# Kernel tuning notes

Measured on AMD Instinct MI355X. Metric: run time of the kernel, lower is better.

Reference implementation:

```python
import jax, jax.numpy as jnp
import numpy as np

CUTOFF = 5.0
NIPSIN = 3
NELE = 4        # natomtype
NWAVE = 10      # ntype: radial params per element
NB, NA, NEIGH = 1, 12000, 64
NPAIR = NA * NEIGH
# index_para: maps 12 angular components (3 p + 9 d) to order index 0/1
INDEX_PARA = np.concatenate([np.full(3 ** i, i - 1, dtype=np.int32) for i in range(1, NIPSIN)])
NANG = INDEX_PARA.shape[0]  # 12


def setup_inputs() -> dict:
    key = jax.random.key(0)
    ks = jax.random.split(key, 8)
    coordinates = jax.random.normal(ks[0], (NB, NA, 3), dtype=jnp.float32)
    numatoms = NA
    atom_index = jax.random.randint(ks[1], (2, NB, NPAIR), 0, NA)
    shifts = jax.random.normal(ks[2], (NB, NPAIR, 3), dtype=jnp.float32) * 0.1
    species = jax.random.randint(ks[3], (NB * NA,), 0, NELE)
    rs = jax.random.uniform(ks[4], (NELE, NWAVE), dtype=jnp.float32) * 4.0
    inta = jax.random.uniform(ks[5], (NELE, NWAVE), dtype=jnp.float32) + 0.2
    params = jax.random.uniform(ks[6], (NELE,), dtype=jnp.float32) * 0.5 + 0.5
    return {"coordinates": coordinates, "numatoms": numatoms, "atom_index": atom_index,
            "shifts": shifts, "species": species, "rs": rs, "inta": inta, "params": params}


def _density(coordinates, atom_index, shifts, species, rs, inta):
    nb, na, _ = coordinates.shape
    coords = coordinates.reshape(-1, 3)
    totnatom = coords.shape[0]
    npair = atom_index.shape[2]
    # flatten pair index lists with per-molecule atom offset (faithful for nb=1)
    ai = jnp.transpose(atom_index, (1, 0, 2)).reshape(2, -1)                 # (2, nb*npair)
    off = jnp.broadcast_to((jnp.arange(nb) * na)[:, None], (nb, npair)).reshape(-1)
    idx12 = ai + off[None, :]
    shift_v = shifts.reshape(-1, 3)
    valid = jnp.all(shift_v > -1e9, axis=-1)                                 # padding mask (all True here)
    dist_vec = coords[idx12[0]] - coords[idx12[1]] + shift_v                 # (P,3)
    d = jnp.linalg.norm(dist_vec, axis=-1)                                   # (P,)
    sp = species[idx12[0]]                                                   # (P,)
    # radial Gaussian * cosine cutoff, params gathered per center-atom type
    fcut = 0.5 * (jnp.cos(jnp.pi * jnp.minimum(d / CUTOFF, 1.0)) + 1.0)
    radial = jnp.exp(-10.0 * inta[sp] * jnp.square(d[:, None] - rs[sp])) * fcut[:, None]
    radial = jnp.where(valid[:, None], radial, 0.0)                          # (P, NWAVE)
    # angular outer products of unit vectors: p (3) then d (9)
    u = dist_vec / d[:, None]
    orbs = []
    orb = jnp.ones((u.shape[0], 1), dtype=u.dtype)
    for _ in range(1, NIPSIN):
        orb = (orb[:, :, None] * u[:, None, :]).reshape(u.shape[0], -1)
        orbs.append(orb)
    angular = jnp.concatenate(orbs, axis=1)                                  # (P, NANG)
    # scatter-reduce into per-(atom, neighbor-type) accumulators, then square
    seg = idx12[0] * NELE + sp
    rd = jax.ops.segment_sum(radial, seg, num_segments=totnatom * NELE)
    rd = jnp.square(rd).reshape(totnatom, NELE, NWAVE)
    oa = (angular[:, :, None] * radial[:, None, :]).reshape(u.shape[0], -1)  # (P, NANG*NWAVE)
    ad = jax.ops.segment_sum(oa, seg, num_segments=totnatom * NELE)
    ad = jnp.square(ad).reshape(totnatom, NELE, NANG, NWAVE)
    # contract angular components of the same order (index_para)
    acc = jnp.zeros((totnatom, NELE, NIPSIN - 1, NWAVE), dtype=ad.dtype)
    acc = acc.at[:, :, jnp.asarray(INDEX_PARA), :].add(ad)
    return jnp.concatenate([rd, acc.reshape(totnatom, NELE, -1)], axis=2)    # (T, NELE, 30)


def reference(coordinates, numatoms, atom_index, shifts, species, rs, inta, params):
    density = _density(coordinates, atom_index, shifts, species, rs, inta)
    density_w = density * params[None, :, None]                 # einsum('ijk,j->ijk')
    g = jnp.einsum('ilj,imj->ijlm', density_w, density_w)       # (T, nfeat, NELE, NELE)
    return jnp.sqrt(g).reshape(g.shape[0], g.shape[1], -1).sum(-1)  # (T, nfeat)
```

## Files before the change

### kernel.cpp

```cpp
#include <hip/hip_runtime.h>
#include <math.h>

#define NA 12000
#define NPAIR 768000
#define NWAVE 10
#define BINS 256
#define APB 47
#define BCAP 4096
#define RCAP 3584
#define PPB 3072

__global__ __launch_bounds__(512) void bin_kernel(
        const float* __restrict__ coords,
        const int* __restrict__ ai0,
        const int* __restrict__ ai1,
        const float* __restrict__ shifts,
        unsigned int* __restrict__ cursor,
        float4* __restrict__ records,
        unsigned char* __restrict__ aloc8) {
    __shared__ unsigned int hist[BINS];
    __shared__ unsigned int gbase[BINS];

    int tid = threadIdx.x;
    if (tid < BINS) hist[tid] = 0u;
    __syncthreads();

    float4 recr[6];
    unsigned int meta[6];
    int pbase = blockIdx.x * PPB;
    #pragma unroll
    for (int r = 0; r < 6; r++) {
        int p  = pbase + r * 512 + tid;
        int a  = ai0[p];
        int j  = ai1[p];
        float sx = shifts[3 * p + 0];
        float sy = shifts[3 * p + 1];
        float sz = shifts[3 * p + 2];
        float dx = coords[3 * a + 0] - coords[3 * j + 0] + sx;
        float dy = coords[3 * a + 1] - coords[3 * j + 1] + sy;
        float dz = coords[3 * a + 2] - coords[3 * j + 2] + sz;
        float d  = sqrtf(dx * dx + dy * dy + dz * dz);
        float tt = fminf(d * 0.2f, 1.0f);
        float fcut = 0.5f * __cosf(3.14159265358979f * tt) + 0.5f;
        if (!((sx > -1e9f) && (sy > -1e9f) && (sz > -1e9f))) fcut = 0.0f;
        unsigned int bin  = (unsigned int)a / 47u;
        unsigned int aloc = (unsigned int)a - bin * 47u;
        recr[r] = make_float4(dx, dy, dz, fcut);
        unsigned int rk = atomicAdd(&hist[bin], 1u);
        meta[r] = (bin << 18) | (aloc << 12) | rk;
    }
    __syncthreads();

    if (tid < BINS) gbase[tid] = atomicAdd(&cursor[tid], hist[tid]);
    __syncthreads();

    #pragma unroll
    for (int r = 0; r < 6; r++) {
        unsigned int bin  = meta[r] >> 18;
        unsigned int aloc = (meta[r] >> 12) & 63u;
        unsigned int gr   = gbase[bin] + (meta[r] & 0xFFFu);
        if (gr < BCAP) {
            unsigned int dg = bin * BCAP + gr;
            records[dg] = recr[r];
            aloc8[dg] = (unsigned char)aloc;
        }
    }
}

__global__ __launch_bounds__(512) void accum_kernel(
        const float4* __restrict__ records,
        const unsigned char* __restrict__ aloc8,
        const int*    __restrict__ species,
        const float*  __restrict__ params,
        const float*  __restrict__ rs,
        const float*  __restrict__ inta,
        const unsigned int* __restrict__ cursor,
        float* __restrict__ out) {
    __shared__ unsigned short idx[RCAP];
    __shared__ float spart[8][APB * 101];
    __shared__ unsigned int hist[APB];
    __shared__ unsigned int offs[APB];
    __shared__ int spl[APB];

    int tid  = threadIdx.x;
    int wv   = tid >> 6;
    int lane = tid & 63;
    int bin  = blockIdx.x;

    if (tid < APB) {
        hist[tid] = 0u;
        int ag = bin * APB + tid;
        spl[tid] = (ag < NA) ? species[ag] : 0;
    }
    __syncthreads();

    unsigned int cnt = cursor[bin];
    if (cnt > RCAP) cnt = RCAP;
    unsigned int base = (unsigned int)bin * BCAP;

    unsigned int pend[7];
    #pragma unroll
    for (int r = 0; r < 7; r++) {
        unsigned int k = (unsigned int)(r * 512 + tid);
        pend[r] = 0xFFFFFFFFu;
        if (k < cnt) {
            unsigned int aloc = aloc8[base + k];
            unsigned int rk = atomicAdd(&hist[aloc], 1u);
            pend[r] = (aloc << 20) | (rk << 12) | k;
        }
    }
    __syncthreads();

    if (wv == 0) {
        unsigned int h0 = (lane < APB) ? hist[lane] : 0u;
        unsigned int h = h0;
        #pragma unroll
        for (int s = 1; s < 64; s <<= 1) {
            unsigned int v = __shfl_up(h, s, 64);
            if (lane >= s) h += v;
        }
        if (lane < APB) offs[lane] = h - h0;
    }
    __syncthreads();

    #pragma unroll
    for (int r = 0; r < 7; r++) {
        if (pend[r] != 0xFFFFFFFFu) {
            unsigned int aloc = pend[r] >> 20;
            unsigned int rk   = (pend[r] >> 12) & 0xFFu;
            unsigned int k    = pend[r] & 0xFFFu;
            idx[offs[aloc] + rk] = (unsigned short)k;
        }
    }
    __syncthreads();

    if (lane < APB) {
        int a = lane;
        unsigned int offa = offs[a];
        unsigned int cnta = hist[a];
        int sp = spl[a];
        float trs[10], tin[10];
        #pragma unroll
        for (int w = 0; w < 10; w++) {
            trs[w] = rs[sp * NWAVE + w];
            tin[w] = -10.0f * inta[sp * NWAVE + w];
        }

        float S[10], P[30], D[60];
        #pragma unroll
        for (int w = 0; w < 10; w++) S[w] = 0.0f;
        #pragma unroll
        for (int c = 0; c < 30; c++) P[c] = 0.0f;
        #pragma unroll
        for (int c = 0; c < 60; c++) D[c] = 0.0f;

        for (unsigned int j = (unsigned int)wv; j < cnta; j += 8) {
            unsigned int k = idx[offa + j];
            float4 rec = records[base + k];
            float fcut = rec.w;
            float d2 = rec.x * rec.x + rec.y * rec.y + rec.z * rec.z;
            float dinv = rsqrtf(fmaxf(d2, 1e-24f));
            float d  = d2 * dinv;
            float ux = rec.x * dinv, uy = rec.y * dinv, uz = rec.z * dinv;
            float uxx = ux * ux, uxy = ux * uy, uxz = ux * uz;
            float uyy = uy * uy, uyz = uy * uz, uzz = uz * uz;
            #pragma unroll
            for (int w = 0; w < 10; w++) {
                float dr = d - trs[w];
                float r  = __expf(tin[w] * dr * dr) * fcut;
                S[w]      += r;
                P[w]      += ux  * r;
                P[10 + w] += uy  * r;
                P[20 + w] += uz  * r;
                D[w]      += uxx * r;
                D[10 + w] += uxy * r;
                D[20 + w] += uxz * r;
                D[30 + w] += uyy * r;
                D[40 + w] += uyz * r;
                D[50 + w] += uzz * r;
            }
        }

        float* row = &spart[wv][a * 101];
        #pragma unroll
        for (int w = 0; w < 10; w++) row[w]      = S[w];
        #pragma unroll
        for (int c = 0; c < 30; c++) row[10 + c] = P[c];
        #pragma unroll
        for (int c = 0; c < 60; c++) row[40 + c] = D[c];
    }
    __syncthreads();

    for (int i = tid; i < APB * 101; i += 512) {
        float s = spart[0][i] + spart[1][i] + spart[2][i] + spart[3][i]
                + spart[4][i] + spart[5][i] + spart[6][i] + spart[7][i];
        spart[0][i] = s;
    }
    __syncthreads();

    for (int v = tid; v < APB * 30; v += 512) {
        int atom = v / 30;
        int c = v - atom * 30;
        int ag = bin * APB + atom;
        if (ag < NA) {
            float pr = params[spl[atom]];
            const float* ap = &spart[0][atom * 101];
            float o;
            if (c < 10) {
                float s = ap[c];
                o = pr * s * s;
            } else if (c < 20) {
                int w = c - 10;
                float a1 = ap[10 + w], b1 = ap[20 + w], c1 = ap[30 + w];
                o = pr * (a1 * a1 + b1 * b1 + c1 * c1);
            } else {
                int w = c - 20;
                float xx = ap[40 + w], xy = ap[50 + w], xz = ap[60 + w];
                float yy = ap[70 + w], yz = ap[80 + w], zz = ap[90 + w];
                o = pr * (xx * xx + yy * yy + zz * zz
                          + 2.0f * (xy * xy + xz * xz + yz * yz));
            }
            out[ag * 30 + c] = o;
        }
    }
}


extern "C" void kernel_launch(void* const* d_in, const int* in_sizes, int n_in,
                              void* d_out, int out_size, void* d_ws, size_t ws_size,
                              hipStream_t stream) {
    const float* coords  = (const float*)d_in[0];
    const int*   aidx    = (const int*)d_in[2];
    const float* shifts  = (const float*)d_in[3];
    const int*   species = (const int*)d_in[4];
    const float* rs      = (const float*)d_in[5];
    const float* inta    = (const float*)d_in[6];
    const float* params  = (const float*)d_in[7];
    float* out = (float*)d_out;

    char* ws = (char*)d_ws;
    float4*        records = (float4*)(ws);
    unsigned int*  cursor  = (unsigned int*)(ws + 16777216);
    unsigned char* aloc8   = (unsigned char*)(ws + 16778240);

    const int* ai0 = aidx;
    const int* ai1 = aidx + NPAIR;

    hipMemsetAsync(cursor, 0, BINS * sizeof(unsigned int), stream);
    bin_kernel<<<NPAIR / PPB, 512, 0, stream>>>(coords, ai0, ai1, shifts,
                                                cursor, records, aloc8);
    accum_kernel<<<BINS, 512, 0, stream>>>(records, aloc8, species, params,
                                           rs, inta, cursor, out);
}
```

Baseline: 111.4 us.

## Sort records by bin in shared memory before global scatter for coalesced writes

The binning kernel now stages each block's computed pair records in LDS, computes an exclusive prefix over the per-bin histogram, and builds a permutation so records are written to global memory in bin-sorted order. Consecutive threads then write contiguous runs within each bin segment, replacing a random scatter of float4 and byte stores. The cost is about 73KB of extra shared memory per block, which lowers occupancy, plus extra barriers and a scan step.

Result: slower. 122.1 us (+9.6%).

```diff
diff --git a/kernel.cpp b/kernel.cpp
--- a/kernel.cpp
+++ b/kernel.cpp
@@ -19,18 +19,23 @@
         float4* __restrict__ records,
         unsigned char* __restrict__ aloc8) {
     __shared__ unsigned int hist[BINS];
+    __shared__ unsigned int excl[BINS];
     __shared__ unsigned int gbase[BINS];
+    __shared__ float4 stage[PPB];
+    __shared__ unsigned char salo[PPB];
+    __shared__ unsigned short inv[PPB];
+    __shared__ unsigned int dest[PPB];
 
     int tid = threadIdx.x;
     if (tid < BINS) hist[tid] = 0u;
     __syncthreads();
 
-    float4 recr[6];
-    unsigned int meta[6];
+    unsigned int binr[6], rankr[6];
     int pbase = blockIdx.x * PPB;
     #pragma unroll
     for (int r = 0; r < 6; r++) {
-        int p  = pbase + r * 512 + tid;
+        int li = r * 512 + tid;
+        int p  = pbase + li;
         int a  = ai0[p];
         int j  = ai1[p];
         float sx = shifts[3 * p + 0];
@@ -45,24 +50,59 @@
         if (!((sx > -1e9f) && (sy > -1e9f) && (sz > -1e9f))) fcut = 0.0f;
         unsigned int bin  = (unsigned int)a / 47u;
         unsigned int aloc = (unsigned int)a - bin * 47u;
-        recr[r] = make_float4(dx, dy, dz, fcut);
+        stage[li] = make_float4(dx, dy, dz, fcut);
+        salo[li]  = (unsigned char)aloc;
         unsigned int rk = atomicAdd(&hist[bin], 1u);
-        meta[r] = (bin << 18) | (aloc << 12) | rk;
-    }
-    __syncthreads();
-
-    if (tid < BINS) gbase[tid] = atomicAdd(&cursor[tid], hist[tid]);
+        binr[r] = bin;
+        rankr[r] = rk;
+    }
+    __syncthreads();
+
+    if (tid < 64) {
+        int l = tid;
+        unsigned int h0 = hist[4 * l + 0];
+        unsigned int h1 = hist[4 * l + 1];
+        unsigned int h2 = hist[4 * l + 2];
+        unsigned int h3 = hist[4 * l + 3];
+        unsigned int mysum = h0 + h1 + h2 + h3;
+        unsigned int incl = mysum;
+        #pragma unroll
+        for (int s = 1; s < 64; s <<= 1) {
+            unsigned int v = __shfl_up(incl, s, 64);
+            if (l >= s) incl += v;
+        }
+        unsigned int b = incl - mysum;
+        excl[4 * l + 0] = b;
+        excl[4 * l + 1] = b + h0;
+        excl[4 * l + 2] = b + h0 + h1;
+        excl[4 * l + 3] = b + h0 + h1 + h2;
+        gbase[4 * l + 0] = atomicAdd(&cursor[4 * l + 0], h0);
+        gbase[4 * l + 1] = atomicAdd(&cursor[4 * l + 1], h1);
+        gbase[4 * l + 2] = atomicAdd(&cursor[4 * l + 2], h2);
+        gbase[4 * l + 3] = atomicAdd(&cursor[4 * l + 3], h3);
+    }
     __syncthreads();
 
     #pragma unroll
     for (int r = 0; r < 6; r++) {
-        unsigned int bin  = meta[r] >> 18;
-        unsigned int aloc = (meta[r] >> 12) & 63u;
-        unsigned int gr   = gbase[bin] + (meta[r] & 0xFFFu);
-        if (gr < BCAP) {
-            unsigned int dg = bin * BCAP + gr;
-            records[dg] = recr[r];
-            aloc8[dg] = (unsigned char)aloc;
+        int li = r * 512 + tid;
+        unsigned int s  = excl[binr[r]] + rankr[r];
+        unsigned int gr = gbase[binr[r]] + rankr[r];
+        inv[s]  = (unsigned short)li;
+        dest[s] = (gr < BCAP) ? (binr[r] * BCAP + gr) : 0xFFFFFFFFu;
+    }
+    __syncthreads();
+
+    #pragma unroll
+    for (int r = 0; r < 6; r++) {
+        int s = r * 512 + tid;
+        int li = inv[s];
+        unsigned int dg = dest[s];
+        float4 rec = stage[li];
+        unsigned char al = salo[li];
+        if (dg != 0xFFFFFFFFu) {
+            records[dg] = rec;
+            aloc8[dg] = al;
         }
     }
 }
```

## Fuse binning and accumulation into one cooperative kernel with grid syncs

Applied to the files above, without the earlier changes.

Merges the memset, binning kernel and accumulation kernel into a single cooperative launch of 256 blocks. A grid-wide sync separates cursor zeroing, binning and accumulation, and the two phases share LDS through a union. Pairs per block change to 3000 so that 256 blocks cover all pairs. This removes two launch gaps and the memset, but adds grid-sync cost. Binning now runs on 256 blocks instead of 250, and occupancy is pinned to one block per CU.

Result: slower. 250.2 us (+124.5%).

```diff
diff --git a/kernel.cpp b/kernel.cpp
--- a/kernel.cpp
+++ b/kernel.cpp
@@ -1,5 +1,8 @@
 #include <hip/hip_runtime.h>
+#include <hip/hip_cooperative_groups.h>
 #include <math.h>
+
+namespace cg = cooperative_groups;
 
 #define NA 12000
 #define NPAIR 768000
@@ -8,89 +11,100 @@
 #define APB 47
 #define BCAP 4096
 #define RCAP 3584
-#define PPB 3072
-
-__global__ __launch_bounds__(512) void bin_kernel(
+#define PPB 3000
+
+struct S1 { unsigned int hist[BINS]; unsigned int gbase[BINS]; };
+struct S2 {
+    unsigned short idx[RCAP];
+    float spart[8][APB * 101];
+    unsigned int hist[APB];
+    unsigned int offs[APB];
+    int spl[APB];
+};
+union SMem { S1 s1; S2 s2; };
+
+__global__ __launch_bounds__(512, 1) void fused_kernel(
         const float* __restrict__ coords,
         const int* __restrict__ ai0,
         const int* __restrict__ ai1,
         const float* __restrict__ shifts,
+        const int* __restrict__ species,
+        const float* __restrict__ params,
+        const float* __restrict__ rs,
+        const float* __restrict__ inta,
         unsigned int* __restrict__ cursor,
         float4* __restrict__ records,
-        unsigned char* __restrict__ aloc8) {
-    __shared__ unsigned int hist[BINS];
-    __shared__ unsigned int gbase[BINS];
-
-    int tid = threadIdx.x;
-    if (tid < BINS) hist[tid] = 0u;
+        unsigned char* __restrict__ aloc8,
+        float* __restrict__ out) {
+    __shared__ SMem sm;
+    cg::grid_group grid = cg::this_grid();
+
+    int tid  = threadIdx.x;
+    int blk  = blockIdx.x;
+    int wv   = tid >> 6;
+    int lane = tid & 63;
+
+    if (tid == 0) cursor[blk] = 0u;
+    grid.sync();
+
+    if (tid < BINS) sm.s1.hist[tid] = 0u;
     __syncthreads();
 
     float4 recr[6];
     unsigned int meta[6];
-    int pbase = blockIdx.x * PPB;
+    int pbase = blk * PPB;
     #pragma unroll
     for (int r = 0; r < 6; r++) {
-        int p  = pbase + r * 512 + tid;
-        int a  = ai0[p];
-        int j  = ai1[p];
-        float sx = shifts[3 * p + 0];
-        float sy = shifts[3 * p + 1];
-        float sz = shifts[3 * p + 2];
-        float dx = coords[3 * a + 0] - coords[3 * j + 0] + sx;
-        float dy = coords[3 * a + 1] - coords[3 * j + 1] + sy;
-        float dz = coords[3 * a + 2] - coords[3 * j + 2] + sz;
-        float d  = sqrtf(dx * dx + dy * dy + dz * dz);
-        float tt = fminf(d * 0.2f, 1.0f);
-        float fcut = 0.5f * __cosf(3.14159265358979f * tt) + 0.5f;
-        if (!((sx > -1e9f) && (sy > -1e9f) && (sz > -1e9f))) fcut = 0.0f;
-        unsigned int bin  = (unsigned int)a / 47u;
-        unsigned int aloc = (unsigned int)a - bin * 47u;
-        recr[r] = make_float4(dx, dy, dz, fcut);
-        unsigned int rk = atomicAdd(&hist[bin], 1u);
-        meta[r] = (bin << 18) | (aloc << 12) | rk;
-    }
-    __syncthreads();
-
-    if (tid < BINS) gbase[tid] = atomicAdd(&cursor[tid], hist[tid]);
+        int li = r * 512 + tid;
+        meta[r] = 0xFFFFFFFFu;
+        if (li < PPB) {
+            int p  = pbase + li;
+            int a  = ai0[p];
+            int j  = ai1[p];
+            float sx = shifts[3 * p + 0];
+            float sy = shifts[3 * p + 1];
+            float sz = shifts[3 * p + 2];
+            float dx = coords[3 * a + 0] - coords[3 * j + 0] + sx;
+            float dy = coords[3 * a + 1] - coords[3 * j + 1] + sy;
+            float dz = coords[3 * a + 2] - coords[3 * j + 2] + sz;
+            float d  = sqrtf(dx * dx + dy * dy + dz * dz);
+            float tt = fminf(d * 0.2f, 1.0f);
+            float fcut = 0.5f * __cosf(3.14159265358979f * tt) + 0.5f;
+            if (!((sx > -1e9f) && (sy > -1e9f) && (sz > -1e9f))) fcut = 0.0f;
+            unsigned int bin  = (unsigned int)a / 47u;
+            unsigned int aloc = (unsigned int)a - bin * 47u;
+            recr[r] = make_float4(dx, dy, dz, fcut);
+            unsigned int rk = atomicAdd(&sm.s1.hist[bin], 1u);
+            meta[r] = (bin << 18) | (aloc << 12) | rk;
+        }
+    }
+    __syncthreads();
+
+    if (tid < BINS) sm.s1.gbase[tid] = atomicAdd(&cursor[tid], sm.s1.hist[tid]);
     __syncthreads();
 
     #pragma unroll
     for (int r = 0; r < 6; r++) {
-        unsigned int bin  = meta[r] >> 18;
-        unsigned int aloc = (meta[r] >> 12) & 63u;
-        unsigned int gr   = gbase[bin] + (meta[r] & 0xFFFu);
-        if (gr < BCAP) {
-            unsigned int dg = bin * BCAP + gr;
-            records[dg] = recr[r];
-            aloc8[dg] = (unsigned char)aloc;
-        }
-    }
-}
-
-__global__ __launch_bounds__(512) void accum_kernel(
-        const float4* __restrict__ records,
-        const unsigned char* __restrict__ aloc8,
-        const int*    __restrict__ species,
-        const float*  __restrict__ params,
-        const float*  __restrict__ rs,
-        const float*  __restrict__ inta,
-        const unsigned int* __restrict__ cursor,
-        float* __restrict__ out) {
-    __shared__ unsigned short idx[RCAP];
-    __shared__ float spart[8][APB * 101];
-    __shared__ unsigned int hist[APB];
-    __shared__ unsigned int offs[APB];
-    __shared__ int spl[APB];
-
-    int tid  = threadIdx.x;
-    int wv   = tid >> 6;
-    int lane = tid & 63;
-    int bin  = blockIdx.x;
-
+        if (meta[r] != 0xFFFFFFFFu) {
+            unsigned int bin  = meta[r] >> 18;
+            unsigned int aloc = (meta[r] >> 12) & 63u;
+            unsigned int gr   = sm.s1.gbase[bin] + (meta[r] & 0xFFFu);
+            if (gr < BCAP) {
+                unsigned int dg = bin * BCAP + gr;
+                records[dg] = recr[r];
+                aloc8[dg] = (unsigned char)aloc;
+            }
+        }
+    }
+
+    __threadfence();
+    grid.sync();
+
+    int bin = blk;
     if (tid < APB) {
-        hist[tid] = 0u;
+        sm.s2.hist[tid] = 0u;
         int ag = bin * APB + tid;
-        spl[tid] = (ag < NA) ? species[ag] : 0;
+        sm.s2.spl[tid] = (ag < NA) ? species[ag] : 0;
     }
     __syncthreads();
 
@@ -105,21 +119,21 @@
         pend[r] = 0xFFFFFFFFu;
         if (k < cnt) {
             unsigned int aloc = aloc8[base + k];
-            unsigned int rk = atomicAdd(&hist[aloc], 1u);
+            unsigned int rk = atomicAdd(&sm.s2.hist[aloc], 1u);
             pend[r] = (aloc << 20) | (rk << 12) | k;
         }
     }
     __syncthreads();
 
     if (wv == 0) {
-        unsigned int h0 = (lane < APB) ? hist[lane] : 0u;
+        unsigned int h0 = (lane < APB) ? sm.s2.hist[lane] : 0u;
         unsigned int h = h0;
         #pragma unroll
         for (int s = 1; s < 64; s <<= 1) {
             unsigned int v = __shfl_up(h, s, 64);
             if (lane >= s) h += v;
         }
-        if (lane < APB) offs[lane] = h - h0;
+        if (lane < APB) sm.s2.offs[lane] = h - h0;
     }
     __syncthreads();
 
@@ -129,16 +143,16 @@
             unsigned int aloc = pend[r] >> 20;
             unsigned int rk   = (pend[r] >> 12) & 0xFFu;
             unsigned int k    = pend[r] & 0xFFFu;
-            idx[offs[aloc] + rk] = (unsigned short)k;
+            sm.s2.idx[sm.s2.offs[aloc] + rk] = (unsigned short)k;
         }
     }
     __syncthreads();
 
     if (lane < APB) {
         int a = lane;
-        unsigned int offa = offs[a];
-        unsigned int cnta = hist[a];
-        int sp = spl[a];
+        unsigned int offa = sm.s2.offs[a];
+        unsigned int cnta = sm.s2.hist[a];
+        int sp = sm.s2.spl[a];
         float trs[10], tin[10];
         #pragma unroll
         for (int w = 0; w < 10; w++) {
@@ -155,7 +169,7 @@
         for (int c = 0; c < 60; c++) D[c] = 0.0f;
 
         for (unsigned int j = (unsigned int)wv; j < cnta; j += 8) {
-            unsigned int k = idx[offa + j];
+            unsigned int k = sm.s2.idx[offa + j];
             float4 rec = records[base + k];
             float fcut = rec.w;
             float d2 = rec.x * rec.x + rec.y * rec.y + rec.z * rec.z;
@@ -181,7 +195,7 @@
             }
         }
 
-        float* row = &spart[wv][a * 101];
+        float* row = &sm.s2.spart[wv][a * 101];
         #pragma unroll
         for (int w = 0; w < 10; w++) row[w]      = S[w];
         #pragma unroll
@@ -192,9 +206,9 @@
     __syncthreads();
 
     for (int i = tid; i < APB * 101; i += 512) {
-        float s = spart[0][i] + spart[1][i] + spart[2][i] + spart[3][i]
-                + spart[4][i] + spart[5][i] + spart[6][i] + spart[7][i];
-        spart[0][i] = s;
+        float s = sm.s2.spart[0][i] + sm.s2.spart[1][i] + sm.s2.spart[2][i] + sm.s2.spart[3][i]
+                + sm.s2.spart[4][i] + sm.s2.spart[5][i] + sm.s2.spart[6][i] + sm.s2.spart[7][i];
+        sm.s2.spart[0][i] = s;
     }
     __syncthreads();
 
@@ -203,8 +217,8 @@
         int c = v - atom * 30;
         int ag = bin * APB + atom;
         if (ag < NA) {
-            float pr = params[spl[atom]];
-            const float* ap = &spart[0][atom * 101];
+            float pr = params[sm.s2.spl[atom]];
+            const float* ap = &sm.s2.spart[0][atom * 101];
             float o;
             if (c < 10) {
                 float s = ap[c];
@@ -246,9 +260,9 @@
     const int* ai0 = aidx;
     const int* ai1 = aidx + NPAIR;
 
-    hipMemsetAsync(cursor, 0, BINS * sizeof(unsigned int), stream);
-    bin_kernel<<<NPAIR / PPB, 512, 0, stream>>>(coords, ai0, ai1, shifts,
-                                                cursor, records, aloc8);
-    accum_kernel<<<BINS, 512, 0, stream>>>(records, aloc8, species, params,
-                                           rs, inta, cursor, out);
+    void* args[] = { (void*)&coords, (void*)&ai0, (void*)&ai1, (void*)&shifts,
+                     (void*)&species, (void*)&params, (void*)&rs, (void*)&inta,
+                     (void*)&cursor, (void*)&records, (void*)&aloc8, (void*)&out };
+    hipLaunchCooperativeKernel((const void*)fused_kernel, dim3(BINS), dim3(512),
+                               args, 0, stream);
 }
```
